# Performance work log

Hardware: AMD Instinct MI355X
Metric: run time of the kernel (lower is better)

## Reference

```python
import jax, jax.numpy as jnp
import numpy as np

D_MODEL = 1024
H = 16
D_K = D_MODEL // H
NEG = -1e9


def setup_inputs() -> dict:
    key = jax.random.key(0)
    ks = jax.random.split(key, 8)
    B, S = 4, 2048
    q = jax.random.normal(ks[0], (B, S, D_MODEL), dtype=jnp.float32)
    k = jax.random.normal(ks[1], (B, S, D_MODEL), dtype=jnp.float32)
    v = jax.random.normal(ks[2], (B, S, D_MODEL), dtype=jnp.float32)
    mask = jax.random.randint(ks[3], (B, S), 0, 2, dtype=jnp.int32)
    scale = 1.0 / np.sqrt(D_MODEL)
    Wq = jax.random.normal(ks[4], (D_MODEL, D_MODEL), dtype=jnp.float32) * scale
    Wk = jax.random.normal(ks[5], (D_MODEL, D_MODEL), dtype=jnp.float32) * scale
    Wv = jax.random.normal(ks[6], (D_MODEL, D_MODEL), dtype=jnp.float32) * scale
    Wo = jax.random.normal(ks[7], (D_MODEL, D_MODEL), dtype=jnp.float32) * scale
    return {"q": q, "k": k, "v": v, "mask": mask,
            "Wq": Wq, "Wk": Wk, "Wv": Wv, "Wo": Wo}


def _split_heads(x):
    # [B,S,d_model] -> [B,H,S,d_k]
    B, S, _ = x.shape
    return x.reshape(B, S, H, D_K).transpose(0, 2, 1, 3)


def reference(q, k, v, mask, Wq, Wk, Wv, Wo):
    # Linear projections (torch Linear: x @ W.T, no bias)
    query = _split_heads(jnp.einsum('bsd,ed->bse', q, Wq))
    key_ = _split_heads(jnp.einsum('bsd,ed->bse', k, Wk))
    value = _split_heads(jnp.einsum('bsd,ed->bse', v, Wv))
    # scaled dot-product attention, manual path
    scores = jnp.einsum('bhqd,bhkd->bhqk', query, key_) / jnp.sqrt(
        jnp.asarray(D_K, dtype=query.dtype))
    m = (mask == 0)[:, None, None, :]  # [B,1,1,S]
    scores = jnp.where(m, jnp.asarray(NEG, dtype=scores.dtype), scores)
    attn = jax.nn.softmax(scores, axis=-1)
    mh = jnp.einsum('bhqk,bhkd->bhqd', attn, value)
    # merge heads -> [B,S,d_model]
    B = mh.shape[0]
    mh = mh.transpose(0, 2, 1, 3).reshape(B, -1, D_MODEL)
    return jnp.einsum('bsd,ed->bse', mh, Wo)
```

## Files before the change

### kernel.cpp

```cpp
#include <hip/hip_runtime.h>
#include <math.h>

typedef __attribute__((ext_vector_type(4))) float f32x4;
typedef __attribute__((ext_vector_type(8))) __bf16 bf16x8;
typedef __attribute__((ext_vector_type(2))) __bf16 bf16x2;

#ifndef __has_builtin
#define __has_builtin(x) 0
#endif

#if __has_builtin(__builtin_amdgcn_exp2f)
#define EXP2F(x) __builtin_amdgcn_exp2f(x)
#else
#define EXP2F(x) exp2f(x)
#endif

__device__ __forceinline__ ushort f2bf(float f) {
  return (ushort)((__float_as_uint(f) + 0x8000u) >> 16);
}

__device__ __forceinline__ uint pack_bf16(float a, float b) {
#if __has_builtin(__builtin_amdgcn_cvt_pk_bf16_f32)
  bf16x2 p = __builtin_amdgcn_cvt_pk_bf16_f32(a, b);
  return __builtin_bit_cast(uint, p);
#elif __has_builtin(__builtin_amdgcn_perm)
  uint au = __float_as_uint(a) + 0x8000u;
  uint bu = __float_as_uint(b) + 0x8000u;
  return __builtin_amdgcn_perm(bu, au, 0x07060302u);
#else
  return (uint)f2bf(a) | ((uint)f2bf(b) << 16);
#endif
}

__device__ __forceinline__ void async_cp16(const void* g, void* l) {
  __builtin_amdgcn_global_load_lds(
      (const __attribute__((address_space(1))) void*)g,
      (__attribute__((address_space(3))) void*)l, 16, 0, 0);
}


__global__ __launch_bounds__(256) void prep_kernel(
    const float* __restrict__ q, const float* __restrict__ k, const float* __restrict__ v,
    const float* __restrict__ Wq, const float* __restrict__ Wk, const float* __restrict__ Wv,
    const float* __restrict__ Wo, const int* __restrict__ mask,
    ushort* qb, ushort* kb, ushort* vb,
    ushort* wqb, ushort* wkb, ushort* wvb, ushort* wob,
    float* bias) {
  int b = blockIdx.x;
  int tid = threadIdx.x;
  if (b < 4096) {
    int j = b >> 10;
    const float* in = j == 0 ? Wq : (j == 1 ? Wk : (j == 2 ? Wv : Wo));
    ushort* out = j == 0 ? wqb : (j == 1 ? wkb : (j == 2 ? wvb : wob));
    int i = (b & 1023) * 256 + tid;
    float4 f = ((const float4*)in)[i];
    uint2 o;
    o.x = pack_bf16(f.x, f.y);
    o.y = pack_bf16(f.z, f.w);
    ((uint2*)out)[i] = o;
  } else if (b < 28672) {
    int bb = b - 4096;
    int j = bb >> 13;
    const float* in = j == 0 ? q : (j == 1 ? k : v);
    ushort* out = j == 0 ? qb : (j == 1 ? kb : vb);
    int i = (bb & 8191) * 256 + tid;
    float4 f = ((const float4*)in)[i];
    uint2 o;
    o.x = pack_bf16(f.x, f.y);
    o.y = pack_bf16(f.z, f.w);
    ((uint2*)out)[i] = o;
  } else {
    int i = (b - 28672) * 256 + tid;
    bias[i] = mask[i] ? 0.0f : -1e9f;
  }
}


__device__ __forceinline__ void gemm_body(const ushort* __restrict__ A,
                                          const ushort* __restrict__ W,
                                          void* __restrict__ Cout, int mode,
                                          int bm, int bn) {
  constexpr int N = 1024, K = 1024;
  __shared__ ushort As[128 * 64];
  __shared__ ushort Bs[128 * 64];
  const int tid = threadIdx.x;
  const int w = tid >> 6, lane = tid & 63;
  const int g = lane >> 4, cc = lane & 15;
  const int wm = (w >> 1) * 64, wn = (w & 1) * 64;

  f32x4 acc[4][4];
#pragma unroll
  for (int i = 0; i < 4; ++i)
#pragma unroll
    for (int j = 0; j < 4; ++j) acc[i][j] = (f32x4)0.0f;

  auto stage = [&](int k0) {
#pragma unroll
    for (int j = 0; j < 4; ++j) {
      int cbase = w * 256 + j * 64;
      int cid = cbase + lane;
      int row = cid & 127, kb = cid >> 7;
      async_cp16(A + (size_t)(bm + row) * K + k0 + kb * 8, &As[cbase * 8]);
      async_cp16(W + (size_t)(bn + row) * K + k0 + kb * 8, &Bs[cbase * 8]);
    }
  };

  stage(0);
  for (int it = 0; it < K / 64; ++it) {
    __syncthreads();
#pragma unroll
    for (int ks = 0; ks < 2; ++ks) {
      bf16x8 af[4], bfr[4];
#pragma unroll
      for (int mi = 0; mi < 4; ++mi)
        af[mi] = *(const bf16x8*)&As[((ks * 4 + g) * 128 + wm + mi * 16 + cc) * 8];
#pragma unroll
      for (int ni = 0; ni < 4; ++ni)
        bfr[ni] = *(const bf16x8*)&Bs[((ks * 4 + g) * 128 + wn + ni * 16 + cc) * 8];
#pragma unroll
      for (int mi = 0; mi < 4; ++mi)
#pragma unroll
        for (int ni = 0; ni < 4; ++ni)
          acc[mi][ni] =
              __builtin_amdgcn_mfma_f32_16x16x32_bf16(af[mi], bfr[ni], acc[mi][ni], 0, 0, 0);
    }
    if (it < K / 64 - 1) {
      __syncthreads();
      stage((it + 1) * 64);
    }
  }

  const float qsc = 0.18033688011112042f;
#pragma unroll
  for (int mi = 0; mi < 4; ++mi) {
#pragma unroll
    for (int ni = 0; ni < 4; ++ni) {
#pragma unroll
      for (int r = 0; r < 4; ++r) {
        int row = bm + wm + mi * 16 + g * 4 + r;
        int col = bn + wn + ni * 16 + cc;
        float val = acc[mi][ni][r];
        if (mode == 0) {
          ((ushort*)Cout)[(size_t)row * N + col] = f2bf(val);
        } else if (mode == 1) {
          ((float*)Cout)[(size_t)row * N + col] = val;
        } else if (mode == 3) {
          ((ushort*)Cout)[(size_t)row * N + col] = f2bf(val * qsc);
        } else {
          int b = row >> 11, s = row & 2047;
          int h = col >> 6, d = col & 63;
          ((ushort*)Cout)[(size_t)((b * 16 + h) * 64 + d) * 2048 + s] = f2bf(val);
        }
      }
    }
  }
}

__global__ __launch_bounds__(256) void qkv_gemm_kernel(const ushort* qb, const ushort* kb,
                                                       const ushort* vb, const ushort* wq,
                                                       const ushort* wk, const ushort* wv,
                                                       ushort* Qp, ushort* Kp, ushort* Vt) {
  int z = blockIdx.z;
  const ushort* A = z == 0 ? qb : (z == 1 ? kb : vb);
  const ushort* W = z == 0 ? wq : (z == 1 ? wk : wv);
  void* C = z == 0 ? (void*)Qp : (z == 1 ? (void*)Kp : (void*)Vt);
  gemm_body(A, W, C, z == 2 ? 2 : (z == 0 ? 3 : 0), blockIdx.y * 128, blockIdx.x * 128);
}

__global__ __launch_bounds__(256) void gemm_wo_kernel(const ushort* A, const ushort* W,
                                                      float* C) {
  gemm_body(A, W, C, 1, blockIdx.y * 128, blockIdx.x * 128);
}

__global__ __launch_bounds__(256, 4) void attn_kernel(const ushort* __restrict__ Qp,
                                                      const ushort* __restrict__ Kp,
                                                      const ushort* __restrict__ Vt,
                                                      const float* __restrict__ bias,
                                                      ushort* __restrict__ mh) {
  constexpr int S = 2048, DM = 1024, DK = 64;
  __shared__ ushort k_lds[64 * 64];
  __shared__ ushort v_lds[64 * 64];
  __shared__ ushort pt_lds[4 * 2176];

  const int bh = blockIdx.x;
  const int qt = blockIdx.y;
  const int b = bh >> 4, h = bh & 15;
  const int tid = threadIdx.x;
  const int w = tid >> 6, lane = tid & 63;
  const int g = lane >> 4, cc = lane & 15;
  ushort* ptw = &pt_lds[w * 2176];

  const int q0 = qt * 128 + w * 32;
  bf16x8 qf[2][2];
#pragma unroll
  for (int ni = 0; ni < 2; ++ni) {
    size_t row = (size_t)(b * S + q0 + ni * 16 + cc);
#pragma unroll
    for (int ks = 0; ks < 2; ++ks)
      qf[ks][ni] = *(const bf16x8*)&Qp[row * DM + h * DK + ks * 32 + g * 8];
  }

  bf16x8 ones;
#pragma unroll
  for (int i = 0; i < 8; ++i) ones[i] = (__bf16)1.0f;

  f32x4 o_acc[4][2];
#pragma unroll
  for (int i = 0; i < 4; ++i)
#pragma unroll
    for (int j = 0; j < 2; ++j) o_acc[i][j] = (f32x4)0.0f;
  f32x4 l_acc[2] = {(f32x4)0.0f, (f32x4)0.0f};
  const float* biasb = bias + b * S;

  for (int kt = 0; kt < S / 64; ++kt) {
    if (kt) __syncthreads();
#pragma unroll
    for (int j = 0; j < 2; ++j) {
      int cb = j * 256 + w * 64;
      int cid = cb + lane;
      async_cp16(Kp + (size_t)(b * S + kt * 64 + (cid & 63)) * DM + h * DK + (cid >> 6) * 8,
                 &k_lds[cb * 8]);
      async_cp16(Vt + (size_t)(bh * DK + (cid & 63)) * S + kt * 64 + (cid >> 6) * 8,
                 &v_lds[cb * 8]);
    }
    __syncthreads();

    f32x4 sacc[4][2];
#pragma unroll
    for (int mi = 0; mi < 4; ++mi)
#pragma unroll
      for (int ni = 0; ni < 2; ++ni) sacc[mi][ni] = (f32x4)0.0f;
    __builtin_amdgcn_s_setprio(1);
#pragma unroll
    for (int ks = 0; ks < 2; ++ks)
#pragma unroll
      for (int mi = 0; mi < 4; ++mi) {
        bf16x8 kf = *(const bf16x8*)&k_lds[((ks * 4 + g) * 64 + mi * 16 + cc) * 8];
        sacc[mi][0] = __builtin_amdgcn_mfma_f32_16x16x32_bf16(kf, qf[ks][0], sacc[mi][0], 0, 0, 0);
        sacc[mi][1] = __builtin_amdgcn_mfma_f32_16x16x32_bf16(kf, qf[ks][1], sacc[mi][1], 0, 0, 0);
      }
    __builtin_amdgcn_s_setprio(0);

#pragma unroll
    for (int mi = 0; mi < 4; ++mi) {
      float4 bv = *(const float4*)&biasb[kt * 64 + mi * 16 + g * 4];
      const float* bvp = &bv.x;
#pragma unroll
      for (int ni = 0; ni < 2; ++ni) {
        float p0 = EXP2F(sacc[mi][ni][0] + bvp[0]);
        float p1 = EXP2F(sacc[mi][ni][1] + bvp[1]);
        float p2 = EXP2F(sacc[mi][ni][2] + bvp[2]);
        float p3 = EXP2F(sacc[mi][ni][3] + bvp[3]);
        uint2 pv;
        pv.x = pack_bf16(p0, p1);
        pv.y = pack_bf16(p2, p3);
        int base = ((mi * 2 + (g >> 1)) * 32 + ni * 16 + cc) * 8 + (g & 1) * 4;
        *(uint2*)&ptw[base] = pv;
      }
    }

    __builtin_amdgcn_s_setprio(1);
#pragma unroll
    for (int ks = 0; ks < 2; ++ks) {
      bf16x8 ptf[2];
#pragma unroll
      for (int ni = 0; ni < 2; ++ni)
        ptf[ni] = *(const bf16x8*)&ptw[((ks * 4 + g) * 32 + ni * 16 + cc) * 8];
      l_acc[0] = __builtin_amdgcn_mfma_f32_16x16x32_bf16(ones, ptf[0], l_acc[0], 0, 0, 0);
      l_acc[1] = __builtin_amdgcn_mfma_f32_16x16x32_bf16(ones, ptf[1], l_acc[1], 0, 0, 0);
#pragma unroll
      for (int md = 0; md < 4; ++md) {
        bf16x8 vf = *(const bf16x8*)&v_lds[((ks * 4 + g) * 64 + md * 16 + cc) * 8];
        o_acc[md][0] = __builtin_amdgcn_mfma_f32_16x16x32_bf16(vf, ptf[0], o_acc[md][0], 0, 0, 0);
        o_acc[md][1] = __builtin_amdgcn_mfma_f32_16x16x32_bf16(vf, ptf[1], o_acc[md][1], 0, 0, 0);
      }
    }
    __builtin_amdgcn_s_setprio(0);
  }

  float rl[2];
#pragma unroll
  for (int ni = 0; ni < 2; ++ni) rl[ni] = 1.0f / l_acc[ni][0];

#pragma unroll
  for (int md = 0; md < 4; ++md)
#pragma unroll
    for (int ni = 0; ni < 2; ++ni) {
      int ql = ni * 16 + cc;
      int dbase = md * 16 + g * 4;
      *(uint*)&ptw[ql * 68 + dbase] =
          pack_bf16(o_acc[md][ni][0] * rl[ni], o_acc[md][ni][1] * rl[ni]);
      *(uint*)&ptw[ql * 68 + dbase + 2] =
          pack_bf16(o_acc[md][ni][2] * rl[ni], o_acc[md][ni][3] * rl[ni]);
    }
#pragma unroll
  for (int pass = 0; pass < 4; ++pass) {
    int ql = pass * 8 + (lane >> 3);
    int dc = lane & 7;
    uint4 val = *(const uint4*)&ptw[ql * 68 + dc * 8];
    *(uint4*)&mh[(size_t)(b * S + q0 + ql) * DM + h * DK + dc * 8] = val;
  }
}


extern "C" void kernel_launch(void* const* d_in, const int* in_sizes, int n_in,
                              void* d_out, int out_size, void* d_ws, size_t ws_size,
                              hipStream_t stream) {
  const float* q = (const float*)d_in[0];
  const float* k = (const float*)d_in[1];
  const float* v = (const float*)d_in[2];
  const int* mask = (const int*)d_in[3];
  const float* Wq = (const float*)d_in[4];
  const float* Wk = (const float*)d_in[5];
  const float* Wv = (const float*)d_in[6];
  const float* Wo = (const float*)d_in[7];

  const size_t MB = 1 << 20;

  char* ws = (char*)d_ws;
  ushort* Qp = (ushort*)(ws);
  ushort* Kp = (ushort*)(ws + 16 * MB);
  ushort* Vt = (ushort*)(ws + 32 * MB);
  ushort* wqb = (ushort*)(ws + 48 * MB);
  ushort* wkb = wqb + (1 << 20);
  ushort* wvb = wkb + (1 << 20);
  ushort* wob = wvb + (1 << 20);
  float* biasbuf = (float*)(ws + 56 * MB);
  ushort* vb = (ushort*)(ws + 57 * MB);
  ushort* mh = vb;
  ushort* qb = (ushort*)d_out;
  ushort* kb = qb + (size_t)8 * 1024 * 1024;

  dim3 blk(256);

  prep_kernel<<<dim3(28704), blk, 0, stream>>>(q, k, v, Wq, Wk, Wv, Wo, mask,
                                               qb, kb, vb, wqb, wkb, wvb, wob, biasbuf);
  qkv_gemm_kernel<<<dim3(8, 64, 3), blk, 0, stream>>>(qb, kb, vb, wqb, wkb, wvb, Qp, Kp, Vt);
  attn_kernel<<<dim3(64, 16), blk, 0, stream>>>(Qp, Kp, Vt, biasbuf, mh);
  gemm_wo_kernel<<<dim3(8, 64), blk, 0, stream>>>(mh, wob, (float*)d_out);
}
```

Measured before the change: 415.3 us.

## Double-buffer GEMM LDS tiles and swizzle block-to-tile mapping

The projection GEMMs now keep two LDS buffers per operand, so the async copy of the next K-slab is issued before the MFMA work on the current slab, removing one barrier per iteration and overlapping loads with compute. Block indices are also remapped so consecutive workgroups cover different M tiles within the same N column group, which changes L2 reuse of weight and activation tiles. The cost is double the LDS footprint (64KB per block), which may lower occupancy. Correctness depends on async_cp16 completing before the barrier, and the block swizzle assumes an 8x64 grid.

```diff
diff --git a/kernel.cpp b/kernel.cpp
--- a/kernel.cpp
+++ b/kernel.cpp
@@ -81,8 +81,8 @@
                                           void* __restrict__ Cout, int mode,
                                           int bm, int bn) {
   constexpr int N = 1024, K = 1024;
-  __shared__ ushort As[128 * 64];
-  __shared__ ushort Bs[128 * 64];
+  __shared__ ushort As[2][128 * 64];
+  __shared__ ushort Bs[2][128 * 64];
   const int tid = threadIdx.x;
   const int w = tid >> 6, lane = tid & 63;
   const int g = lane >> 4, cc = lane & 15;
@@ -94,29 +94,31 @@
 #pragma unroll
     for (int j = 0; j < 4; ++j) acc[i][j] = (f32x4)0.0f;
 
-  auto stage = [&](int k0) {
+  auto stage = [&](int k0, int buf) {
 #pragma unroll
     for (int j = 0; j < 4; ++j) {
       int cbase = w * 256 + j * 64;
       int cid = cbase + lane;
       int row = cid & 127, kb = cid >> 7;
-      async_cp16(A + (size_t)(bm + row) * K + k0 + kb * 8, &As[cbase * 8]);
-      async_cp16(W + (size_t)(bn + row) * K + k0 + kb * 8, &Bs[cbase * 8]);
+      async_cp16(A + (size_t)(bm + row) * K + k0 + kb * 8, &As[buf][cbase * 8]);
+      async_cp16(W + (size_t)(bn + row) * K + k0 + kb * 8, &Bs[buf][cbase * 8]);
     }
   };
 
-  stage(0);
+  stage(0, 0);
+  __syncthreads();
   for (int it = 0; it < K / 64; ++it) {
-    __syncthreads();
+    const int cur = it & 1;
+    if (it < K / 64 - 1) stage((it + 1) * 64, cur ^ 1);
 #pragma unroll
     for (int ks = 0; ks < 2; ++ks) {
       bf16x8 af[4], bfr[4];
 #pragma unroll
       for (int mi = 0; mi < 4; ++mi)
-        af[mi] = *(const bf16x8*)&As[((ks * 4 + g) * 128 + wm + mi * 16 + cc) * 8];
+        af[mi] = *(const bf16x8*)&As[cur][((ks * 4 + g) * 128 + wm + mi * 16 + cc) * 8];
 #pragma unroll
       for (int ni = 0; ni < 4; ++ni)
-        bfr[ni] = *(const bf16x8*)&Bs[((ks * 4 + g) * 128 + wn + ni * 16 + cc) * 8];
+        bfr[ni] = *(const bf16x8*)&Bs[cur][((ks * 4 + g) * 128 + wn + ni * 16 + cc) * 8];
 #pragma unroll
       for (int mi = 0; mi < 4; ++mi)
 #pragma unroll
@@ -124,10 +126,7 @@
           acc[mi][ni] =
               __builtin_amdgcn_mfma_f32_16x16x32_bf16(af[mi], bfr[ni], acc[mi][ni], 0, 0, 0);
     }
-    if (it < K / 64 - 1) {
-      __syncthreads();
-      stage((it + 1) * 64);
-    }
+    __syncthreads();
   }
 
   const float qsc = 0.18033688011112042f;
@@ -156,6 +155,13 @@
   }
 }
 
+__device__ __forceinline__ void swz_tile(int* bm, int* bn) {
+  int l = blockIdx.x + (blockIdx.y << 3);
+  int t = ((l & 7) << 6) + (l >> 3);
+  *bn = (t & 7) * 128;
+  *bm = (t >> 3) * 128;
+}
+
 __global__ __launch_bounds__(256) void qkv_gemm_kernel(const ushort* qb, const ushort* kb,
                                                        const ushort* vb, const ushort* wq,
                                                        const ushort* wk, const ushort* wv,
@@ -164,12 +170,16 @@
   const ushort* A = z == 0 ? qb : (z == 1 ? kb : vb);
   const ushort* W = z == 0 ? wq : (z == 1 ? wk : wv);
   void* C = z == 0 ? (void*)Qp : (z == 1 ? (void*)Kp : (void*)Vt);
-  gemm_body(A, W, C, z == 2 ? 2 : (z == 0 ? 3 : 0), blockIdx.y * 128, blockIdx.x * 128);
+  int bm, bn;
+  swz_tile(&bm, &bn);
+  gemm_body(A, W, C, z == 2 ? 2 : (z == 0 ? 3 : 0), bm, bn);
 }
 
 __global__ __launch_bounds__(256) void gemm_wo_kernel(const ushort* A, const ushort* W,
                                                       float* C) {
-  gemm_body(A, W, C, 1, blockIdx.y * 128, blockIdx.x * 128);
+  int bm, bn;
+  swz_tile(&bm, &bn);
+  gemm_body(A, W, C, 1, bm, bn);
 }
 
 __global__ __launch_bounds__(256, 4) void attn_kernel(const ushort* __restrict__ Qp,
```

Measured after the change: 438.8 us. +5.7%, slower.
